# Performance work log

Hardware: AMD Instinct MI355X
Metric: run time of the kernel (lower is better)

Reference implementation:

```python
import jax, jax.numpy as jnp
import numpy as np

DIM = 192
SHIFT = 3
PAD = SHIFT // 2  # 1
EPS = 1e-5


def conv1x1(x, w, b):
    # 1x1x1 Conv3d == channel matmul. x: (B,C,D,H,W), w: (O,C), b: (O,)
    return jnp.einsum('bcdhw,oc->bodhw', x, w) + b[None, :, None, None, None]


def group_norm1(x, w, b):
    # GroupNorm(1, C): normalize over (C,D,H,W) per sample, per-channel affine.
    mu = x.mean(axis=(1, 2, 3, 4), keepdims=True)
    var = x.var(axis=(1, 2, 3, 4), keepdims=True)
    xn = (x - mu) * jax.lax.rsqrt(var + EPS)
    return xn * w[None, :, None, None, None] + b[None, :, None, None, None]


def axial_shift(x, axis):
    # reflect-pad all 3 spatial dims, roll channel-chunks along `axis`, crop back.
    R = x.shape[-1]
    xp = jnp.pad(x, ((0, 0), (0, 0), (PAD, PAD), (PAD, PAD), (PAD, PAD)), mode='reflect')
    chunks = jnp.split(xp, SHIFT, axis=1)
    rolled = [jnp.roll(c, s, axis=axis) for c, s in zip(chunks, range(-PAD, PAD + 1))]
    xc = jnp.concatenate(rolled, axis=1)
    return xc[:, :, PAD:PAD + R, PAD:PAD + R, PAD:PAD + R]


def setup_inputs() -> dict:
    key = jax.random.key(0)
    ks = jax.random.split(key, 16)
    B, C, R = 8, DIM, 32
    x = jax.random.normal(ks[0], (B, C, R, R, R), dtype=jnp.float32)
    wmat = lambda k: jax.random.normal(k, (C, C), dtype=jnp.float32) * 0.05
    vec = lambda k: jax.random.normal(k, (C,), dtype=jnp.float32) * 0.05
    return {
        'x': x,
        'w1': wmat(ks[1]), 'b1': vec(ks[2]),
        'n1w': jnp.ones((C,), jnp.float32), 'n1b': jnp.zeros((C,), jnp.float32),
        'w21': wmat(ks[3]), 'b21': vec(ks[4]),
        'w22': wmat(ks[5]), 'b22': vec(ks[6]),
        'w23': wmat(ks[7]), 'b23': vec(ks[8]),
        'n2w': jnp.ones((C,), jnp.float32), 'n2b': jnp.zeros((C,), jnp.float32),
        'w3': wmat(ks[9]), 'b3': vec(ks[10]),
    }


def reference(x, w1, b1, n1w, n1b, w21, b21, w22, b22, w23, b23, n2w, n2b, w3, b3):
    h = conv1x1(x, w1, b1)
    h = group_norm1(h, n1w, n1b)
    h = jax.nn.gelu(h, approximate=False)
    h = axial_shift(h, axis=3)
    h = conv1x1(h, w22, b22)
    h = axial_shift(h, axis=2)
    h = conv1x1(h, w21, b21)
    h = axial_shift(h, axis=4)
    h = conv1x1(h, w23, b23)
    h = jax.nn.gelu(h, approximate=False)
    h = group_norm1(h, n2w, n2b)
    h = conv1x1(h, w3, b3)
    return h
```

## Files before the change

kernel.cpp:

```cpp
#include <hip/hip_runtime.h>
#include <math.h>

#define NCH 192
#define NB 8
#define SPAT 32768
#define TILES_PER_B 512
#define NBLK (NB * TILES_PER_B)
#define NELEM_PER_B ((size_t)NCH * SPAT)

typedef short s16x8 __attribute__((ext_vector_type(8)));
typedef float f32x4 __attribute__((ext_vector_type(4)));

__device__ __forceinline__ float bf2f(unsigned short h) {
  return __uint_as_float(((unsigned)h) << 16);
}
__device__ __forceinline__ unsigned short f2bf(float f) {
  unsigned u = __float_as_uint(f);
  u += 0x7FFF + ((u >> 16) & 1);
  return (unsigned short)(u >> 16);
}
__device__ __forceinline__ unsigned cvt_pk(float lo, float hi) {
  unsigned r;
  asm("v_cvt_pk_bf16_f32 %0, %1, %2" : "=v"(r) : "v"(lo), "v"(hi));
  return r;
}

__device__ __forceinline__ float gelu_f(float x) {
  float x2 = x * x;
  float z2 = x * fmaf(x2, 0.0713548163f, 1.5957769100f);
  float e = __expf(z2);
  float r = __builtin_amdgcn_rcpf(e + 1.0f);
  return fmaf(-r, x, x);
}

__device__ __forceinline__ int rshift(int i, int c) {
  int j = i - (c - 1);
  j = (j < 0) ? 1 : j;
  j = (j > 31) ? 30 : j;
  return j;
}

__device__ __forceinline__ int lds_off(int c, int p, int u) {
  return (c * 64 + p) * 128 + 16 * (((u >> 3) ^ (p & 7) ^ ((p >> 3) & 7)) & 7) + 2 * (u & 7);
}

template <int SHIFTW>
__device__ __forceinline__ void do_gemm48(const char* __restrict__ B,
                                          const unsigned short* __restrict__ wm,
                                          int wave, int col, int kg,
                                          f32x4 acc[3][4]) {
  const unsigned short* wp = wm + (wave * 48 + col) * NCH + kg * 8;
  s16x8 afc[3], afn[3];
#pragma unroll
  for (int r = 0; r < 3; ++r) afc[r] = *(const s16x8*)(wp + r * 16 * NCH);
#pragma unroll
  for (int ks = 0; ks < 6; ++ks) {
    if (ks < 5) {
#pragma unroll
      for (int r = 0; r < 3; ++r)
        afn[r] = *(const s16x8*)(wp + (ks + 1) * 32 + r * 16 * NCH);
    }
    int k0 = ks * 32 + kg * 8;
    int c = k0 >> 6, u = k0 & 63;
    s16x8 bf[4];
#pragma unroll
    for (int m = 0; m < 4; ++m) {
      int p = m * 16 + col;
      int ps = SHIFTW ? ((p & 32) | rshift(p & 31, c)) : p;
      bf[m] = *(const s16x8*)(B + lds_off(c, ps, u));
    }
#pragma unroll
    for (int r = 0; r < 3; ++r)
#pragma unroll
      for (int m = 0; m < 4; ++m)
        acc[r][m] = __builtin_amdgcn_mfma_f32_16x16x32_bf16(afc[r], bf[m], acc[r][m], 0, 0, 0);
#pragma unroll
    for (int r = 0; r < 3; ++r) afc[r] = afn[r];
  }
}

__device__ __forceinline__ void stats_reduce(float ssum, float ssq, int wave, int lane,
                                             float* red, float* partials, int blk) {
#pragma unroll
  for (int off = 1; off < 64; off <<= 1) {
    ssum += __shfl_xor(ssum, off, 64);
    ssq += __shfl_xor(ssq, off, 64);
  }
  if (lane == 0) { red[wave * 2] = ssum; red[wave * 2 + 1] = ssq; }
  __syncthreads();
  if (wave == 0 && lane == 0) {
    partials[blk * 2] = red[0] + red[2] + red[4] + red[6];
    partials[blk * 2 + 1] = red[1] + red[3] + red[5] + red[7];
  }
}

__device__ __forceinline__ void store_tile(const char* __restrict__ L, char* __restrict__ ob,
                                           int tid) {
  int G = tid & 7;
#pragma unroll
  for (int j = 0; j < 6; ++j) {
    const int c = j >> 1;
    int p = (j & 1) * 32 + (tid >> 3);
    s16x8 v = *(const s16x8*)(L + lds_off(c, p, G * 8));
    *(s16x8*)(ob + (size_t)p * 384 + (c * 8 + G) * 16) = v;
  }
}

__global__ __launch_bounds__(256, 4)
void pass1(const float* __restrict__ x, const unsigned short* __restrict__ w1b,
           const float* __restrict__ b1, unsigned short* __restrict__ out,
           float* __restrict__ partials) {
  __shared__ __align__(16) char B[3 * 64 * 128];
  __shared__ float red[8];
  int blk = blockIdx.x, b = blk >> 9, p0 = (blk & 511) * 64;
  int tid = threadIdx.x, wave = tid >> 6, lane = tid & 63;
  int col = lane & 15, kg = lane >> 4;

  const float* xb = x + (size_t)b * NELEM_PER_B + p0;
  int q = tid & 15;
#pragma unroll
  for (int j = 0; j < 6; ++j) {
    int chp = j * 16 + (tid >> 4);
    int ch0 = 2 * chp;
    int cc = chp >> 5, u0 = ch0 & 63;
    const float* s0 = xb + (size_t)ch0 * SPAT + 4 * q;
    f32x4 a = *(const f32x4*)s0;
    f32x4 c2 = *(const f32x4*)(s0 + SPAT);
#pragma unroll
    for (int i = 0; i < 4; ++i)
      *(unsigned*)(B + lds_off(cc, 4 * q + i, u0)) = cvt_pk(a[i], c2[i]);
  }
  __syncthreads();

  f32x4 acc[3][4] = {};
  do_gemm48<0>(B, w1b, wave, col, kg, acc);

  float ssum = 0.f, ssq = 0.f;
  __syncthreads();
#pragma unroll
  for (int r = 0; r < 3; ++r) {
    int rowb = wave * 48 + r * 16 + kg * 4;
    f32x4 bs = *(const f32x4*)(b1 + rowb);
#pragma unroll
    for (int m = 0; m < 4; ++m) {
      int p = m * 16 + col;
      float v0 = acc[r][m][0] + bs[0], v1 = acc[r][m][1] + bs[1];
      float v2 = acc[r][m][2] + bs[2], v3 = acc[r][m][3] + bs[3];
      ssum += (v0 + v1) + (v2 + v3);
      ssq = fmaf(v0, v0, fmaf(v1, v1, fmaf(v2, v2, fmaf(v3, v3, ssq))));
      uint2 pk; pk.x = cvt_pk(v0, v1); pk.y = cvt_pk(v2, v3);
      *(uint2*)(B + lds_off(rowb >> 6, p, rowb & 63)) = pk;
    }
  }
  __syncthreads();
  store_tile(B, (char*)out + ((size_t)b * SPAT + p0) * 384, tid);
  stats_reduce(ssum, ssq, wave, lane, red, partials, blk);
}

__global__ __launch_bounds__(256, 4)
void pass2a(const unsigned short* __restrict__ in, const unsigned short* __restrict__ w22b,
            const float* __restrict__ b22, unsigned short* __restrict__ out,
            const unsigned short* __restrict__ ACbf) {
  __shared__ __align__(16) char B[3 * 64 * 128];
  int blk = blockIdx.x, b = blk >> 9, p0 = (blk & 511) * 64;
  int tid = threadIdx.x, wave = tid >> 6, lane = tid & 63;
  int col = lane & 15, kg = lane >> 4;

  const char* ib = (const char*)in + (size_t)b * SPAT * 384;
  const unsigned short* acb = ACbf + b * 2 * NCH;
  int G = tid & 7;
#pragma unroll
  for (int j = 0; j < 6; ++j) {
    const int c = j >> 1;
    int p = (j & 1) * 32 + (tid >> 3);
    int h = ((p0 + p) >> 5) & 31;
    int sp = (p0 + p) + (rshift(h, c) - h) * 32;
    s16x8 v = *(const s16x8*)(ib + (size_t)sp * 384 + (c * 8 + G) * 16);
    s16x8 aA = *(const s16x8*)(acb + c * 64 + G * 8);
    s16x8 aC = *(const s16x8*)(acb + NCH + c * 64 + G * 8);
    unsigned w[4];
#pragma unroll
    for (int i = 0; i < 4; ++i) {
      float f0 = gelu_f(fmaf(bf2f((unsigned short)v[2 * i]), bf2f((unsigned short)aA[2 * i]),
                             bf2f((unsigned short)aC[2 * i])));
      float f1 = gelu_f(fmaf(bf2f((unsigned short)v[2 * i + 1]), bf2f((unsigned short)aA[2 * i + 1]),
                             bf2f((unsigned short)aC[2 * i + 1])));
      w[i] = cvt_pk(f0, f1);
    }
    *(uint2*)(B + lds_off(c, p, G * 8)) = make_uint2(w[0], w[1]);
    *(uint2*)(B + lds_off(c, p, G * 8 + 4)) = make_uint2(w[2], w[3]);
  }
  __syncthreads();

  f32x4 acc[3][4] = {};
  do_gemm48<0>(B, w22b, wave, col, kg, acc);
  __syncthreads();
#pragma unroll
  for (int r = 0; r < 3; ++r) {
    int rowb = wave * 48 + r * 16 + kg * 4;
    f32x4 bs = *(const f32x4*)(b22 + rowb);
#pragma unroll
    for (int m = 0; m < 4; ++m) {
      int p = m * 16 + col;
      uint2 pk;
      pk.x = cvt_pk(acc[r][m][0] + bs[0], acc[r][m][1] + bs[1]);
      pk.y = cvt_pk(acc[r][m][2] + bs[2], acc[r][m][3] + bs[3]);
      *(uint2*)(B + lds_off(rowb >> 6, p, rowb & 63)) = pk;
    }
  }
  __syncthreads();
  store_tile(B, (char*)out + ((size_t)b * SPAT + p0) * 384, tid);
}

__global__ __launch_bounds__(256, 4)
void pass2bc(const unsigned short* __restrict__ in, const unsigned short* __restrict__ w21b,
             const float* __restrict__ b21, const unsigned short* __restrict__ w23b,
             const float* __restrict__ b23, unsigned short* __restrict__ out,
             float* __restrict__ partials) {
  __shared__ __align__(16) char B[3 * 64 * 128];
  __shared__ float red[8];
  int blk = blockIdx.x, b = blk >> 9, p0 = (blk & 511) * 64;
  int tid = threadIdx.x, wave = tid >> 6, lane = tid & 63;
  int col = lane & 15, kg = lane >> 4;

  int d = p0 >> 10;
  int soff[3];
#pragma unroll
  for (int c = 0; c < 3; ++c) soff[c] = (rshift(d, c) - d) * 1024;

  const char* ib = (const char*)in + (size_t)b * SPAT * 384;
  int G = tid & 7;
#pragma unroll
  for (int j = 0; j < 6; ++j) {
    const int c = j >> 1;
    int p = (j & 1) * 32 + (tid >> 3);
    s16x8 v = *(const s16x8*)(ib + (size_t)(p0 + p + soff[c]) * 384 + (c * 8 + G) * 16);
    *(s16x8*)(B + lds_off(c, p, G * 8)) = v;
  }
  __syncthreads();

  f32x4 acc[3][4] = {};
  do_gemm48<0>(B, w21b, wave, col, kg, acc);
  __syncthreads();
#pragma unroll
  for (int r = 0; r < 3; ++r) {
    int rowb = wave * 48 + r * 16 + kg * 4;
    f32x4 bs = *(const f32x4*)(b21 + rowb);
#pragma unroll
    for (int m = 0; m < 4; ++m) {
      int p = m * 16 + col;
      uint2 pk;
      pk.x = cvt_pk(acc[r][m][0] + bs[0], acc[r][m][1] + bs[1]);
      pk.y = cvt_pk(acc[r][m][2] + bs[2], acc[r][m][3] + bs[3]);
      *(uint2*)(B + lds_off(rowb >> 6, p, rowb & 63)) = pk;
    }
  }
  __syncthreads();

#pragma unroll
  for (int r = 0; r < 3; ++r)
#pragma unroll
    for (int m = 0; m < 4; ++m) acc[r][m] = (f32x4){0.f, 0.f, 0.f, 0.f};
  do_gemm48<1>(B, w23b, wave, col, kg, acc);
  __syncthreads();

  float ssum = 0.f, ssq = 0.f;
#pragma unroll
  for (int r = 0; r < 3; ++r) {
    int rowb = wave * 48 + r * 16 + kg * 4;
    f32x4 bs = *(const f32x4*)(b23 + rowb);
#pragma unroll
    for (int m = 0; m < 4; ++m) {
      int p = m * 16 + col;
      float v0 = gelu_f(acc[r][m][0] + bs[0]), v1 = gelu_f(acc[r][m][1] + bs[1]);
      float v2 = gelu_f(acc[r][m][2] + bs[2]), v3 = gelu_f(acc[r][m][3] + bs[3]);
      ssum += (v0 + v1) + (v2 + v3);
      ssq = fmaf(v0, v0, fmaf(v1, v1, fmaf(v2, v2, fmaf(v3, v3, ssq))));
      uint2 pk; pk.x = cvt_pk(v0, v1); pk.y = cvt_pk(v2, v3);
      *(uint2*)(B + lds_off(rowb >> 6, p, rowb & 63)) = pk;
    }
  }
  __syncthreads();
  store_tile(B, (char*)out + ((size_t)b * SPAT + p0) * 384, tid);
  stats_reduce(ssum, ssq, wave, lane, red, partials, blk);
}

__global__ __launch_bounds__(256, 4)
void pass3(const unsigned short* __restrict__ in, const unsigned short* __restrict__ w3e,
           const float* __restrict__ b3e, float* __restrict__ outf) {
  __shared__ __align__(16) char B[3 * 64 * 128];
  int blk = blockIdx.x, b = blk >> 9, p0 = (blk & 511) * 64;
  int tid = threadIdx.x, wave = tid >> 6, lane = tid & 63;
  int col = lane & 15, kg = lane >> 4;

  const char* ib = (const char*)in + (size_t)b * SPAT * 384;
  int G = tid & 7;
#pragma unroll
  for (int j = 0; j < 6; ++j) {
    const int c = j >> 1;
    int p = (j & 1) * 32 + (tid >> 3);
    s16x8 v = *(const s16x8*)(ib + (size_t)(p0 + p) * 384 + (c * 8 + G) * 16);
    *(s16x8*)(B + lds_off(c, p, G * 8)) = v;
  }
  __syncthreads();

  f32x4 acc[3][4] = {};
  do_gemm48<0>(B, w3e + (size_t)b * NCH * NCH, wave, col, kg, acc);

  const float* bb = b3e + b * NCH;
#pragma unroll
  for (int r = 0; r < 3; ++r) {
    int rowb = wave * 48 + r * 16 + kg * 4;
    f32x4 bs = *(const f32x4*)(bb + rowb);
#pragma unroll
    for (int m = 0; m < 4; ++m) {
      int p = p0 + m * 16 + col;
#pragma unroll
      for (int j = 0; j < 4; ++j)
        outf[((size_t)b * NCH + rowb + j) * SPAT + p] = acc[r][m][j] + bs[j];
    }
  }
}

__global__ void stats_finalize(const float* __restrict__ partials,
                               const float* __restrict__ nw, const float* __restrict__ nb,
                               float* __restrict__ AC, unsigned short* __restrict__ ACbf) {
  int b = blockIdx.x, tid = threadIdx.x;
  __shared__ float s0[256], s1[256];
  float a = 0.f, c = 0.f;
  for (int i = tid; i < TILES_PER_B; i += 256) {
    a += partials[(b * TILES_PER_B + i) * 2];
    c += partials[(b * TILES_PER_B + i) * 2 + 1];
  }
  s0[tid] = a; s1[tid] = c;
  __syncthreads();
  for (int st = 128; st > 0; st >>= 1) {
    if (tid < st) { s0[tid] += s0[tid + st]; s1[tid] += s1[tid + st]; }
    __syncthreads();
  }
  float inv_n = 1.0f / (float)NELEM_PER_B;
  float mu = s0[0] * inv_n;
  float var = s1[0] * inv_n - mu * mu;
  float rs = rsqrtf(var + 1e-5f);
  if (tid < NCH) {
    float A = rs * nw[tid];
    float C = nb[tid] - mu * A;
    AC[b * 2 * NCH + tid] = A;
    AC[b * 2 * NCH + NCH + tid] = C;
    ACbf[b * 2 * NCH + tid] = f2bf(A);
    ACbf[b * 2 * NCH + NCH + tid] = f2bf(C);
  }
}

__global__ void prep_weights(const float* __restrict__ w1, const float* __restrict__ w21,
                             const float* __restrict__ w22, const float* __restrict__ w23,
                             unsigned short* __restrict__ wb) {
  int i = blockIdx.x * 256 + threadIdx.x;
  if (i >= 4 * NCH * NCH) return;
  int m = i / (NCH * NCH), r = i % (NCH * NCH);
  const float* src = (m == 0) ? w1 : (m == 1) ? w22 : (m == 2) ? w21 : w23;
  wb[i] = f2bf(src[r]);
}

__global__ void prep_w3(const float* __restrict__ w3, const float* __restrict__ b3,
                        const float* __restrict__ AC2,
                        unsigned short* __restrict__ w3e, float* __restrict__ b3e) {
  int b = blockIdx.x, o = threadIdx.x;
  if (o >= NCH) return;
  const float* A = AC2 + b * 2 * NCH;
  const float* C = A + NCH;
  float s = b3[o];
  for (int c = 0; c < NCH; ++c) {
    float w = w3[o * NCH + c];
    w3e[((size_t)b * NCH + o) * NCH + c] = f2bf(w * A[c]);
    s = fmaf(w, C[c], s);
  }
  b3e[b * NCH + o] = s;
}

extern "C" void kernel_launch(void* const* d_in, const int* in_sizes, int n_in,
                              void* d_out, int out_size, void* d_ws, size_t ws_size,
                              hipStream_t stream) {
  const float* x   = (const float*)d_in[0];
  const float* w1  = (const float*)d_in[1];
  const float* b1  = (const float*)d_in[2];
  const float* n1w = (const float*)d_in[3];
  const float* n1b = (const float*)d_in[4];
  const float* w21 = (const float*)d_in[5];
  const float* b21 = (const float*)d_in[6];
  const float* w22 = (const float*)d_in[7];
  const float* b22 = (const float*)d_in[8];
  const float* w23 = (const float*)d_in[9];
  const float* b23 = (const float*)d_in[10];
  const float* n2w = (const float*)d_in[11];
  const float* n2b = (const float*)d_in[12];
  const float* w3  = (const float*)d_in[13];
  const float* b3  = (const float*)d_in[14];

  char* ws = (char*)d_ws;
  size_t off = 0;
  unsigned short* wb = (unsigned short*)(ws + off); off += (size_t)4 * NCH * NCH * 2;
  off = (off + 255) & ~(size_t)255;
  unsigned short* w3e = (unsigned short*)(ws + off); off += (size_t)NB * NCH * NCH * 2;
  off = (off + 255) & ~(size_t)255;
  float* b3e = (float*)(ws + off); off += NB * NCH * 4;
  float* AC1 = (float*)(ws + off); off += NB * 2 * NCH * 4;
  float* AC2 = (float*)(ws + off); off += NB * 2 * NCH * 4;
  unsigned short* ACbf1 = (unsigned short*)(ws + off); off += NB * 2 * NCH * 2;
  unsigned short* ACbf2 = (unsigned short*)(ws + off); off += NB * 2 * NCH * 2;
  off = (off + 255) & ~(size_t)255;
  float* part1 = (float*)(ws + off); off += (size_t)NBLK * 2 * 4;
  float* part2 = (float*)(ws + off); off += (size_t)NBLK * 2 * 4;
  off = (off + 255) & ~(size_t)255;
  unsigned short* R1 = (unsigned short*)(ws + off);
  unsigned short* R2 = (unsigned short*)d_out;

  prep_weights<<<(4 * NCH * NCH + 255) / 256, 256, 0, stream>>>(w1, w21, w22, w23, wb);

  pass1<<<NBLK, 256, 0, stream>>>(x, wb + 0 * NCH * NCH, b1, R1, part1);
  stats_finalize<<<NB, 256, 0, stream>>>(part1, n1w, n1b, AC1, ACbf1);

  pass2a<<<NBLK, 256, 0, stream>>>(R1, wb + 1 * NCH * NCH, b22, R2, ACbf1);

  pass2bc<<<NBLK, 256, 0, stream>>>(R2, wb + 2 * NCH * NCH, b21,
                                    wb + 3 * NCH * NCH, b23, R1, part2);
  stats_finalize<<<NB, 256, 0, stream>>>(part2, n2w, n2b, AC2, ACbf2);
  prep_w3<<<NB, NCH, 0, stream>>>(w3, b3, AC2, w3e, b3e);

  pass3<<<NBLK, 256, 0, stream>>>(R1, w3e, b3e, (float*)d_out);
}
```

Measured before the change: 334.5 us.

## Process four tiles per block with register-prefetched, double-buffered LDS pipeline

The shift/GEMM passes (2a, 2bc, 3) are merged into one templated persistent-style kernel, and pass3 gets the same treatment. Each block now handles four 64-voxel tiles and loads the next tile's global data into registers while the current tile's MFMA GEMM runs, using two LDS buffers and custom barriers. The aim is to hide global load latency and cut block launch and tail overhead. In exchange the grid is four times smaller, LDS per block doubles, and the launch-bounds occupancy hint of 4 is dropped, so fewer waves may be resident.

```diff
diff --git a/kernel.cpp b/kernel.cpp
--- a/kernel.cpp
+++ b/kernel.cpp
@@ -5,7 +5,9 @@
 #define NB 8
 #define SPAT 32768
 #define TILES_PER_B 512
-#define NBLK (NB * TILES_PER_B)
+#define NBLK1 (NB * TILES_PER_B)
+#define TPW 4
+#define NBLKP (NB * (TILES_PER_B / TPW))
 #define NELEM_PER_B ((size_t)NCH * SPAT)
 
 typedef short s16x8 __attribute__((ext_vector_type(8)));
@@ -42,6 +44,21 @@
 
 __device__ __forceinline__ int lds_off(int c, int p, int u) {
   return (c * 64 + p) * 128 + 16 * (((u >> 3) ^ (p & 7) ^ ((p >> 3) & 7)) & 7) + 2 * (u & 7);
+}
+
+__device__ __forceinline__ void bar_lgkm() {
+  __builtin_amdgcn_sched_barrier(0);
+  asm volatile("s_waitcnt lgkmcnt(0)" ::: "memory");
+  __builtin_amdgcn_s_barrier();
+  asm volatile("" ::: "memory");
+  __builtin_amdgcn_sched_barrier(0);
+}
+__device__ __forceinline__ void bar_plain() {
+  __builtin_amdgcn_sched_barrier(0);
+  asm volatile("" ::: "memory");
+  __builtin_amdgcn_s_barrier();
+  asm volatile("" ::: "memory");
+  __builtin_amdgcn_sched_barrier(0);
 }
 
 template <int SHIFTW>
@@ -79,6 +96,62 @@
   }
 }
 
+template <int AX>
+__device__ __forceinline__ void stage_load(const char* __restrict__ ib, int p0, int tid,
+                                           s16x8 vr[6]) {
+#pragma unroll
+  for (int j = 0; j < 6; ++j) {
+    const int c = j >> 1;
+    int p = (j & 1) * 32 + (tid >> 3);
+    int G = tid & 7;
+    int pp = p0 + p, sp;
+    if (AX == 0) sp = pp;
+    else if (AX == 3) { int h = (pp >> 5) & 31; sp = pp + (rshift(h, c) - h) * 32; }
+    else            { int d = pp >> 10;       sp = pp + (rshift(d, c) - d) * 1024; }
+    vr[j] = *(const s16x8*)(ib + (size_t)sp * 384 + (c * 8 + G) * 16);
+  }
+}
+
+template <int FUSE>
+__device__ __forceinline__ void stage_write(char* __restrict__ B, int tid, const s16x8 vr[6],
+                                            const unsigned short* __restrict__ acb) {
+#pragma unroll
+  for (int j = 0; j < 6; ++j) {
+    const int c = j >> 1;
+    int p = (j & 1) * 32 + (tid >> 3);
+    int G = tid & 7;
+    if (FUSE) {
+      s16x8 aA = *(const s16x8*)(acb + c * 64 + G * 8);
+      s16x8 aC = *(const s16x8*)(acb + NCH + c * 64 + G * 8);
+      unsigned w[4];
+#pragma unroll
+      for (int i = 0; i < 4; ++i) {
+        float f0 = gelu_f(fmaf(bf2f((unsigned short)vr[j][2 * i]), bf2f((unsigned short)aA[2 * i]),
+                               bf2f((unsigned short)aC[2 * i])));
+        float f1 = gelu_f(fmaf(bf2f((unsigned short)vr[j][2 * i + 1]), bf2f((unsigned short)aA[2 * i + 1]),
+                               bf2f((unsigned short)aC[2 * i + 1])));
+        w[i] = cvt_pk(f0, f1);
+      }
+      *(uint2*)(B + lds_off(c, p, G * 8)) = make_uint2(w[0], w[1]);
+      *(uint2*)(B + lds_off(c, p, G * 8 + 4)) = make_uint2(w[2], w[3]);
+    } else {
+      *(s16x8*)(B + lds_off(c, p, G * 8)) = vr[j];
+    }
+  }
+}
+
+__device__ __forceinline__ void store_tile(const char* __restrict__ L, char* __restrict__ ob,
+                                           int tid) {
+  int G = tid & 7;
+#pragma unroll
+  for (int j = 0; j < 6; ++j) {
+    const int c = j >> 1;
+    int p = (j & 1) * 32 + (tid >> 3);
+    s16x8 v = *(const s16x8*)(L + lds_off(c, p, G * 8));
+    *(s16x8*)(ob + (size_t)p * 384 + (c * 8 + G) * 16) = v;
+  }
+}
+
 __device__ __forceinline__ void stats_reduce(float ssum, float ssq, int wave, int lane,
                                              float* red, float* partials, int blk) {
 #pragma unroll
@@ -91,18 +164,6 @@
   if (wave == 0 && lane == 0) {
     partials[blk * 2] = red[0] + red[2] + red[4] + red[6];
     partials[blk * 2 + 1] = red[1] + red[3] + red[5] + red[7];
-  }
-}
-
-__device__ __forceinline__ void store_tile(const char* __restrict__ L, char* __restrict__ ob,
-                                           int tid) {
-  int G = tid & 7;
-#pragma unroll
-  for (int j = 0; j < 6; ++j) {
-    const int c = j >> 1;
-    int p = (j & 1) * 32 + (tid >> 3);
-    s16x8 v = *(const s16x8*)(L + lds_off(c, p, G * 8));
-    *(s16x8*)(ob + (size_t)p * 384 + (c * 8 + G) * 16) = v;
   }
 }
 
@@ -157,180 +218,141 @@
   stats_reduce(ssum, ssq, wave, lane, red, partials, blk);
 }
 
-__global__ __launch_bounds__(256, 4)
-void pass2a(const unsigned short* __restrict__ in, const unsigned short* __restrict__ w22b,
-            const float* __restrict__ b22, unsigned short* __restrict__ out,
-            const unsigned short* __restrict__ ACbf) {
-  __shared__ __align__(16) char B[3 * 64 * 128];
-  int blk = blockIdx.x, b = blk >> 9, p0 = (blk & 511) * 64;
+template <int AX, int FUSE, int CHAIN, int EPI2>
+__global__ __launch_bounds__(256)
+void pipe_pass(const unsigned short* __restrict__ in, const unsigned short* __restrict__ wA,
+               const float* __restrict__ bA, const unsigned short* __restrict__ wB,
+               const float* __restrict__ bB, unsigned short* __restrict__ out,
+               float* __restrict__ partials, const unsigned short* __restrict__ ACbf) {
+  __shared__ __align__(16) char buf[2][3 * 64 * 128];
+  __shared__ float red[8];
+  int blk = blockIdx.x, b = blk / (TILES_PER_B / TPW);
+  int ti0 = (blk % (TILES_PER_B / TPW)) * TPW;
   int tid = threadIdx.x, wave = tid >> 6, lane = tid & 63;
   int col = lane & 15, kg = lane >> 4;
 
   const char* ib = (const char*)in + (size_t)b * SPAT * 384;
-  const unsigned short* acb = ACbf + b * 2 * NCH;
-  int G = tid & 7;
-#pragma unroll
-  for (int j = 0; j < 6; ++j) {
-    const int c = j >> 1;
-    int p = (j & 1) * 32 + (tid >> 3);
-    int h = ((p0 + p) >> 5) & 31;
-    int sp = (p0 + p) + (rshift(h, c) - h) * 32;
-    s16x8 v = *(const s16x8*)(ib + (size_t)sp * 384 + (c * 8 + G) * 16);
-    s16x8 aA = *(const s16x8*)(acb + c * 64 + G * 8);
-    s16x8 aC = *(const s16x8*)(acb + NCH + c * 64 + G * 8);
-    unsigned w[4];
-#pragma unroll
-    for (int i = 0; i < 4; ++i) {
-      float f0 = gelu_f(fmaf(bf2f((unsigned short)v[2 * i]), bf2f((unsigned short)aA[2 * i]),
-                             bf2f((unsigned short)aC[2 * i])));
-      float f1 = gelu_f(fmaf(bf2f((unsigned short)v[2 * i + 1]), bf2f((unsigned short)aA[2 * i + 1]),
-                             bf2f((unsigned short)aC[2 * i + 1])));
-      w[i] = cvt_pk(f0, f1);
-    }
-    *(uint2*)(B + lds_off(c, p, G * 8)) = make_uint2(w[0], w[1]);
-    *(uint2*)(B + lds_off(c, p, G * 8 + 4)) = make_uint2(w[2], w[3]);
-  }
-  __syncthreads();
-
-  f32x4 acc[3][4] = {};
-  do_gemm48<0>(B, w22b, wave, col, kg, acc);
-  __syncthreads();
-#pragma unroll
-  for (int r = 0; r < 3; ++r) {
-    int rowb = wave * 48 + r * 16 + kg * 4;
-    f32x4 bs = *(const f32x4*)(b22 + rowb);
-#pragma unroll
-    for (int m = 0; m < 4; ++m) {
-      int p = m * 16 + col;
-      uint2 pk;
-      pk.x = cvt_pk(acc[r][m][0] + bs[0], acc[r][m][1] + bs[1]);
-      pk.y = cvt_pk(acc[r][m][2] + bs[2], acc[r][m][3] + bs[3]);
-      *(uint2*)(B + lds_off(rowb >> 6, p, rowb & 63)) = pk;
-    }
-  }
-  __syncthreads();
-  store_tile(B, (char*)out + ((size_t)b * SPAT + p0) * 384, tid);
-}
-
-__global__ __launch_bounds__(256, 4)
-void pass2bc(const unsigned short* __restrict__ in, const unsigned short* __restrict__ w21b,
-             const float* __restrict__ b21, const unsigned short* __restrict__ w23b,
-             const float* __restrict__ b23, unsigned short* __restrict__ out,
-             float* __restrict__ partials) {
-  __shared__ __align__(16) char B[3 * 64 * 128];
-  __shared__ float red[8];
-  int blk = blockIdx.x, b = blk >> 9, p0 = (blk & 511) * 64;
+  const unsigned short* acb = FUSE ? (ACbf + b * 2 * NCH) : nullptr;
+  float ssum = 0.f, ssq = 0.f;
+
+  s16x8 vr[6];
+  stage_load<AX>(ib, ti0 * 64, tid, vr);
+
+#pragma unroll
+  for (int t = 0; t < TPW; ++t) {
+    char* W = buf[t & 1];
+    int p0 = (ti0 + t) * 64;
+
+    stage_write<FUSE>(W, tid, vr, acb);
+    if (t + 1 < TPW) stage_load<AX>(ib, (ti0 + t + 1) * 64, tid, vr);
+    bar_lgkm();
+
+    f32x4 acc[3][4] = {};
+    do_gemm48<0>(W, wA, wave, col, kg, acc);
+    bar_plain();
+
+    if constexpr (CHAIN) {
+#pragma unroll
+      for (int r = 0; r < 3; ++r) {
+        int rowb = wave * 48 + r * 16 + kg * 4;
+        f32x4 bs = *(const f32x4*)(bA + rowb);
+#pragma unroll
+        for (int m = 0; m < 4; ++m) {
+          int p = m * 16 + col;
+          uint2 pk;
+          pk.x = cvt_pk(acc[r][m][0] + bs[0], acc[r][m][1] + bs[1]);
+          pk.y = cvt_pk(acc[r][m][2] + bs[2], acc[r][m][3] + bs[3]);
+          *(uint2*)(W + lds_off(rowb >> 6, p, rowb & 63)) = pk;
+        }
+      }
+      bar_lgkm();
+#pragma unroll
+      for (int r = 0; r < 3; ++r)
+#pragma unroll
+        for (int m = 0; m < 4; ++m) acc[r][m] = (f32x4){0.f, 0.f, 0.f, 0.f};
+      do_gemm48<1>(W, wB, wave, col, kg, acc);
+      bar_plain();
+    }
+
+    const float* bfin = CHAIN ? bB : bA;
+#pragma unroll
+    for (int r = 0; r < 3; ++r) {
+      int rowb = wave * 48 + r * 16 + kg * 4;
+      f32x4 bs = *(const f32x4*)(bfin + rowb);
+#pragma unroll
+      for (int m = 0; m < 4; ++m) {
+        int p = m * 16 + col;
+        float v0 = acc[r][m][0] + bs[0], v1 = acc[r][m][1] + bs[1];
+        float v2 = acc[r][m][2] + bs[2], v3 = acc[r][m][3] + bs[3];
+        if (EPI2) {
+          v0 = gelu_f(v0); v1 = gelu_f(v1); v2 = gelu_f(v2); v3 = gelu_f(v3);
+          ssum += (v0 + v1) + (v2 + v3);
+          ssq = fmaf(v0, v0, fmaf(v1, v1, fmaf(v2, v2, fmaf(v3, v3, ssq))));
+        }
+        uint2 pk; pk.x = cvt_pk(v0, v1); pk.y = cvt_pk(v2, v3);
+        *(uint2*)(W + lds_off(rowb >> 6, p, rowb & 63)) = pk;
+      }
+    }
+    bar_lgkm();
+    store_tile(W, (char*)out + ((size_t)b * SPAT + p0) * 384, tid);
+  }
+
+  if (EPI2) stats_reduce(ssum, ssq, wave, lane, red, partials, blk);
+}
+
+__global__ __launch_bounds__(256)
+void pass3(const unsigned short* __restrict__ in, const unsigned short* __restrict__ w3e,
+           const float* __restrict__ b3e, float* __restrict__ outf) {
+  __shared__ __align__(16) char buf[2][3 * 64 * 128];
+  int blk = blockIdx.x, b = blk / (TILES_PER_B / TPW);
+  int ti0 = (blk % (TILES_PER_B / TPW)) * TPW;
   int tid = threadIdx.x, wave = tid >> 6, lane = tid & 63;
   int col = lane & 15, kg = lane >> 4;
 
-  int d = p0 >> 10;
-  int soff[3];
-#pragma unroll
-  for (int c = 0; c < 3; ++c) soff[c] = (rshift(d, c) - d) * 1024;
-
   const char* ib = (const char*)in + (size_t)b * SPAT * 384;
-  int G = tid & 7;
-#pragma unroll
-  for (int j = 0; j < 6; ++j) {
-    const int c = j >> 1;
-    int p = (j & 1) * 32 + (tid >> 3);
-    s16x8 v = *(const s16x8*)(ib + (size_t)(p0 + p + soff[c]) * 384 + (c * 8 + G) * 16);
-    *(s16x8*)(B + lds_off(c, p, G * 8)) = v;
-  }
-  __syncthreads();
-
-  f32x4 acc[3][4] = {};
-  do_gemm48<0>(B, w21b, wave, col, kg, acc);
-  __syncthreads();
-#pragma unroll
-  for (int r = 0; r < 3; ++r) {
-    int rowb = wave * 48 + r * 16 + kg * 4;
-    f32x4 bs = *(const f32x4*)(b21 + rowb);
-#pragma unroll
-    for (int m = 0; m < 4; ++m) {
-      int p = m * 16 + col;
-      uint2 pk;
-      pk.x = cvt_pk(acc[r][m][0] + bs[0], acc[r][m][1] + bs[1]);
-      pk.y = cvt_pk(acc[r][m][2] + bs[2], acc[r][m][3] + bs[3]);
-      *(uint2*)(B + lds_off(rowb >> 6, p, rowb & 63)) = pk;
-    }
-  }
-  __syncthreads();
-
-#pragma unroll
-  for (int r = 0; r < 3; ++r)
-#pragma unroll
-    for (int m = 0; m < 4; ++m) acc[r][m] = (f32x4){0.f, 0.f, 0.f, 0.f};
-  do_gemm48<1>(B, w23b, wave, col, kg, acc);
-  __syncthreads();
-
-  float ssum = 0.f, ssq = 0.f;
-#pragma unroll
-  for (int r = 0; r < 3; ++r) {
-    int rowb = wave * 48 + r * 16 + kg * 4;
-    f32x4 bs = *(const f32x4*)(b23 + rowb);
-#pragma unroll
-    for (int m = 0; m < 4; ++m) {
-      int p = m * 16 + col;
-      float v0 = gelu_f(acc[r][m][0] + bs[0]), v1 = gelu_f(acc[r][m][1] + bs[1]);
-      float v2 = gelu_f(acc[r][m][2] + bs[2]), v3 = gelu_f(acc[r][m][3] + bs[3]);
-      ssum += (v0 + v1) + (v2 + v3);
-      ssq = fmaf(v0, v0, fmaf(v1, v1, fmaf(v2, v2, fmaf(v3, v3, ssq))));
-      uint2 pk; pk.x = cvt_pk(v0, v1); pk.y = cvt_pk(v2, v3);
-      *(uint2*)(B + lds_off(rowb >> 6, p, rowb & 63)) = pk;
-    }
-  }
-  __syncthreads();
-  store_tile(B, (char*)out + ((size_t)b * SPAT + p0) * 384, tid);
-  stats_reduce(ssum, ssq, wave, lane, red, partials, blk);
-}
-
-__global__ __launch_bounds__(256, 4)
-void pass3(const unsigned short* __restrict__ in, const unsigned short* __restrict__ w3e,
-           const float* __restrict__ b3e, float* __restrict__ outf) {
-  __shared__ __align__(16) char B[3 * 64 * 128];
-  int blk = blockIdx.x, b = blk >> 9, p0 = (blk & 511) * 64;
-  int tid = threadIdx.x, wave = tid >> 6, lane = tid & 63;
-  int col = lane & 15, kg = lane >> 4;
-
-  const char* ib = (const char*)in + (size_t)b * SPAT * 384;
-  int G = tid & 7;
-#pragma unroll
-  for (int j = 0; j < 6; ++j) {
-    const int c = j >> 1;
-    int p = (j & 1) * 32 + (tid >> 3);
-    s16x8 v = *(const s16x8*)(ib + (size_t)(p0 + p) * 384 + (c * 8 + G) * 16);
-    *(s16x8*)(B + lds_off(c, p, G * 8)) = v;
-  }
-  __syncthreads();
-
-  f32x4 acc[3][4] = {};
-  do_gemm48<0>(B, w3e + (size_t)b * NCH * NCH, wave, col, kg, acc);
-
+  const unsigned short* wbase = w3e + (size_t)b * NCH * NCH;
   const float* bb = b3e + b * NCH;
-#pragma unroll
-  for (int r = 0; r < 3; ++r) {
-    int rowb = wave * 48 + r * 16 + kg * 4;
-    f32x4 bs = *(const f32x4*)(bb + rowb);
-#pragma unroll
-    for (int m = 0; m < 4; ++m) {
-      int p = p0 + m * 16 + col;
-#pragma unroll
-      for (int j = 0; j < 4; ++j)
-        outf[((size_t)b * NCH + rowb + j) * SPAT + p] = acc[r][m][j] + bs[j];
+
+  s16x8 vr[6];
+  stage_load<0>(ib, ti0 * 64, tid, vr);
+
+#pragma unroll
+  for (int t = 0; t < TPW; ++t) {
+    char* W = buf[t & 1];
+    int p0 = (ti0 + t) * 64;
+    stage_write<0>(W, tid, vr, nullptr);
+    if (t + 1 < TPW) stage_load<0>(ib, (ti0 + t + 1) * 64, tid, vr);
+    bar_lgkm();
+
+    f32x4 acc[3][4] = {};
+    do_gemm48<0>(W, wbase, wave, col, kg, acc);
+    bar_lgkm();
+
+#pragma unroll
+    for (int r = 0; r < 3; ++r) {
+      int rowb = wave * 48 + r * 16 + kg * 4;
+      f32x4 bs = *(const f32x4*)(bb + rowb);
+#pragma unroll
+      for (int m = 0; m < 4; ++m) {
+        int p = p0 + m * 16 + col;
+#pragma unroll
+        for (int j = 0; j < 4; ++j)
+          outf[((size_t)b * NCH + rowb + j) * SPAT + p] = acc[r][m][j] + bs[j];
+      }
     }
   }
 }
 
 __global__ void stats_finalize(const float* __restrict__ partials,
                                const float* __restrict__ nw, const float* __restrict__ nb,
-                               float* __restrict__ AC, unsigned short* __restrict__ ACbf) {
+                               float* __restrict__ AC, unsigned short* __restrict__ ACbf,
+                               int nper) {
   int b = blockIdx.x, tid = threadIdx.x;
   __shared__ float s0[256], s1[256];
   float a = 0.f, c = 0.f;
-  for (int i = tid; i < TILES_PER_B; i += 256) {
-    a += partials[(b * TILES_PER_B + i) * 2];
-    c += partials[(b * TILES_PER_B + i) * 2 + 1];
+  for (int i = tid; i < nper; i += 256) {
+    a += partials[(b * nper + i) * 2];
+    c += partials[(b * nper + i) * 2 + 1];
   }
   s0[tid] = a; s1[tid] = c;
   __syncthreads();
@@ -409,23 +431,24 @@
   unsigned short* ACbf1 = (unsigned short*)(ws + off); off += NB * 2 * NCH * 2;
   unsigned short* ACbf2 = (unsigned short*)(ws + off); off += NB * 2 * NCH * 2;
   off = (off + 255) & ~(size_t)255;
-  float* part1 = (float*)(ws + off); off += (size_t)NBLK * 2 * 4;
-  float* part2 = (float*)(ws + off); off += (size_t)NBLK * 2 * 4;
+  float* part1 = (float*)(ws + off); off += (size_t)NBLK1 * 2 * 4;
+  float* part2 = (float*)(ws + off); off += (size_t)NBLKP * 2 * 4;
   off = (off + 255) & ~(size_t)255;
   unsigned short* R1 = (unsigned short*)(ws + off);
   unsigned short* R2 = (unsigned short*)d_out;
 
   prep_weights<<<(4 * NCH * NCH + 255) / 256, 256, 0, stream>>>(w1, w21, w22, w23, wb);
 
-  pass1<<<NBLK, 256, 0, stream>>>(x, wb + 0 * NCH * NCH, b1, R1, part1);
-  stats_finalize<<<NB, 256, 0, stream>>>(part1, n1w, n1b, AC1, ACbf1);
-
-  pass2a<<<NBLK, 256, 0, stream>>>(R1, wb + 1 * NCH * NCH, b22, R2, ACbf1);
-
-  pass2bc<<<NBLK, 256, 0, stream>>>(R2, wb + 2 * NCH * NCH, b21,
-                                    wb + 3 * NCH * NCH, b23, R1, part2);
-  stats_finalize<<<NB, 256, 0, stream>>>(part2, n2w, n2b, AC2, ACbf2);
+  pass1<<<NBLK1, 256, 0, stream>>>(x, wb + 0 * NCH * NCH, b1, R1, part1);
+  stats_finalize<<<NB, 256, 0, stream>>>(part1, n1w, n1b, AC1, ACbf1, TILES_PER_B);
+
+  pipe_pass<3, 1, 0, 0><<<NBLKP, 256, 0, stream>>>(
+      R1, wb + 1 * NCH * NCH, b22, nullptr, nullptr, R2, nullptr, ACbf1);
+
+  pipe_pass<2, 0, 1, 1><<<NBLKP, 256, 0, stream>>>(
+      R2, wb + 2 * NCH * NCH, b21, wb + 3 * NCH * NCH, b23, R1, part2, nullptr);
+  stats_finalize<<<NB, 256, 0, stream>>>(part2, n2w, n2b, AC2, ACbf2, TILES_PER_B / TPW);
   prep_w3<<<NB, NCH, 0, stream>>>(w3, b3, AC2, w3e, b3e);
 
-  pass3<<<NBLK, 256, 0, stream>>>(R1, w3e, b3e, (float*)d_out);
-}
+  pass3<<<NBLKP, 256, 0, stream>>>(R1, w3e, b3e, (float*)d_out);
+}
```

New measurement: 343.4 us. 1.03x slower.

## Replace pass2a and pass3 with single-wave 16-pixel-tile GEMM kernel

Applied to the files above, without the earlier changes.

Introduces a templated single-wavefront kernel that processes 16 spatial positions per block, with all 192 output channels computed by one wave, and uses it in place of the 256-thread, 64-position pass2a and pass3 kernels. The aim is more, smaller blocks with no __syncthreads, for better latency hiding and finer load balance. In exchange, every wave re-reads the full 192x192 weight matrix from global or cache for only 16 columns, which greatly raises weight traffic per output. The fp32 output store in pass3 also becomes narrower (16 contiguous floats per row).

```diff
diff --git a/kernel.cpp b/kernel.cpp
--- a/kernel.cpp
+++ b/kernel.cpp
@@ -5,7 +5,8 @@
 #define NB 8
 #define SPAT 32768
 #define TILES_PER_B 512
-#define NBLK (NB * TILES_PER_B)
+#define NBLK1 (NB * TILES_PER_B)
+#define NTLP (NB * 2048)
 #define NELEM_PER_B ((size_t)NCH * SPAT)
 
 typedef short s16x8 __attribute__((ext_vector_type(8)));
@@ -42,6 +43,9 @@
 
 __device__ __forceinline__ int lds_off(int c, int p, int u) {
   return (c * 64 + p) * 128 + 16 * (((u >> 3) ^ (p & 7) ^ ((p >> 3) & 7)) & 7) + 2 * (u & 7);
+}
+__device__ __forceinline__ int lds_off16(int c, int p, int u) {
+  return (c * 16 + p) * 128 + 16 * (((u >> 3) ^ (p & 7) ^ ((p >> 3) & 7)) & 7) + 2 * (u & 7);
 }
 
 template <int SHIFTW>
@@ -79,21 +83,6 @@
   }
 }
 
-__device__ __forceinline__ void stats_reduce(float ssum, float ssq, int wave, int lane,
-                                             float* red, float* partials, int blk) {
-#pragma unroll
-  for (int off = 1; off < 64; off <<= 1) {
-    ssum += __shfl_xor(ssum, off, 64);
-    ssq += __shfl_xor(ssq, off, 64);
-  }
-  if (lane == 0) { red[wave * 2] = ssum; red[wave * 2 + 1] = ssq; }
-  __syncthreads();
-  if (wave == 0 && lane == 0) {
-    partials[blk * 2] = red[0] + red[2] + red[4] + red[6];
-    partials[blk * 2 + 1] = red[1] + red[3] + red[5] + red[7];
-  }
-}
-
 __device__ __forceinline__ void store_tile(const char* __restrict__ L, char* __restrict__ ob,
                                            int tid) {
   int G = tid & 7;
@@ -103,6 +92,21 @@
     int p = (j & 1) * 32 + (tid >> 3);
     s16x8 v = *(const s16x8*)(L + lds_off(c, p, G * 8));
     *(s16x8*)(ob + (size_t)p * 384 + (c * 8 + G) * 16) = v;
+  }
+}
+
+__device__ __forceinline__ void stats_reduce(float ssum, float ssq, int wave, int lane,
+                                             float* red, float* partials, int blk) {
+#pragma unroll
+  for (int off = 1; off < 64; off <<= 1) {
+    ssum += __shfl_xor(ssum, off, 64);
+    ssq += __shfl_xor(ssq, off, 64);
+  }
+  if (lane == 0) { red[wave * 2] = ssum; red[wave * 2 + 1] = ssq; }
+  __syncthreads();
+  if (wave == 0 && lane == 0) {
+    partials[blk * 2] = red[0] + red[2] + red[4] + red[6];
+    partials[blk * 2 + 1] = red[1] + red[3] + red[5] + red[7];
   }
 }
 
@@ -157,59 +161,100 @@
   stats_reduce(ssum, ssq, wave, lane, red, partials, blk);
 }
 
-__global__ __launch_bounds__(256, 4)
-void pass2a(const unsigned short* __restrict__ in, const unsigned short* __restrict__ w22b,
-            const float* __restrict__ b22, unsigned short* __restrict__ out,
-            const unsigned short* __restrict__ ACbf) {
-  __shared__ __align__(16) char B[3 * 64 * 128];
-  int blk = blockIdx.x, b = blk >> 9, p0 = (blk & 511) * 64;
-  int tid = threadIdx.x, wave = tid >> 6, lane = tid & 63;
-  int col = lane & 15, kg = lane >> 4;
+template <int AX, int FUSE, int PERB, int OUTF>
+__global__ __launch_bounds__(64, 4)
+void tlp_pass(const unsigned short* __restrict__ in,
+              const unsigned short* __restrict__ wmat,
+              const float* __restrict__ bias,
+              void* __restrict__ outv,
+              const unsigned short* __restrict__ ACbf) {
+  __shared__ __align__(16) char B[3 * 16 * 128];
+  int blk = blockIdx.x;
+  int b = blk >> 11;
+  int p0 = (blk & 2047) * 16;
+  int lane = threadIdx.x & 63;
+  int col = lane & 15, kg = lane >> 4, G = lane & 7;
 
   const char* ib = (const char*)in + (size_t)b * SPAT * 384;
-  const unsigned short* acb = ACbf + b * 2 * NCH;
-  int G = tid & 7;
+  const unsigned short* wbase = wmat + (PERB ? (size_t)b * NCH * NCH : 0);
+  const float* bbase = bias + (PERB ? b * NCH : 0);
+  const unsigned short* acb = FUSE ? (ACbf + b * 2 * NCH) : nullptr;
+
 #pragma unroll
   for (int j = 0; j < 6; ++j) {
     const int c = j >> 1;
-    int p = (j & 1) * 32 + (tid >> 3);
-    int h = ((p0 + p) >> 5) & 31;
-    int sp = (p0 + p) + (rshift(h, c) - h) * 32;
+    int p = (j & 1) * 8 + (lane >> 3);
+    int pp = p0 + p;
+    int sp = pp;
+    if (AX == 3) { int h = (pp >> 5) & 31; sp = pp + (rshift(h, c) - h) * 32; }
     s16x8 v = *(const s16x8*)(ib + (size_t)sp * 384 + (c * 8 + G) * 16);
-    s16x8 aA = *(const s16x8*)(acb + c * 64 + G * 8);
-    s16x8 aC = *(const s16x8*)(acb + NCH + c * 64 + G * 8);
-    unsigned w[4];
-#pragma unroll
-    for (int i = 0; i < 4; ++i) {
-      float f0 = gelu_f(fmaf(bf2f((unsigned short)v[2 * i]), bf2f((unsigned short)aA[2 * i]),
-                             bf2f((unsigned short)aC[2 * i])));
-      float f1 = gelu_f(fmaf(bf2f((unsigned short)v[2 * i + 1]), bf2f((unsigned short)aA[2 * i + 1]),
-                             bf2f((unsigned short)aC[2 * i + 1])));
-      w[i] = cvt_pk(f0, f1);
-    }
-    *(uint2*)(B + lds_off(c, p, G * 8)) = make_uint2(w[0], w[1]);
-    *(uint2*)(B + lds_off(c, p, G * 8 + 4)) = make_uint2(w[2], w[3]);
-  }
-  __syncthreads();
-
-  f32x4 acc[3][4] = {};
-  do_gemm48<0>(B, w22b, wave, col, kg, acc);
-  __syncthreads();
-#pragma unroll
-  for (int r = 0; r < 3; ++r) {
-    int rowb = wave * 48 + r * 16 + kg * 4;
-    f32x4 bs = *(const f32x4*)(b22 + rowb);
-#pragma unroll
-    for (int m = 0; m < 4; ++m) {
-      int p = m * 16 + col;
+    if (FUSE) {
+      s16x8 aA = *(const s16x8*)(acb + c * 64 + G * 8);
+      s16x8 aC = *(const s16x8*)(acb + NCH + c * 64 + G * 8);
+      unsigned w[4];
+#pragma unroll
+      for (int i = 0; i < 4; ++i) {
+        float f0 = gelu_f(fmaf(bf2f((unsigned short)v[2 * i]),
+                               bf2f((unsigned short)aA[2 * i]),
+                               bf2f((unsigned short)aC[2 * i])));
+        float f1 = gelu_f(fmaf(bf2f((unsigned short)v[2 * i + 1]),
+                               bf2f((unsigned short)aA[2 * i + 1]),
+                               bf2f((unsigned short)aC[2 * i + 1])));
+        w[i] = cvt_pk(f0, f1);
+      }
+      *(uint2*)(B + lds_off16(c, p, G * 8)) = make_uint2(w[0], w[1]);
+      *(uint2*)(B + lds_off16(c, p, G * 8 + 4)) = make_uint2(w[2], w[3]);
+    } else {
+      *(s16x8*)(B + lds_off16(c, p, G * 8)) = v;
+    }
+  }
+
+  f32x4 acc[12] = {};
+#pragma unroll
+  for (int rb = 0; rb < 2; ++rb) {
+#pragma unroll
+    for (int ks = 0; ks < 6; ++ks) {
+      int k0 = ks * 32 + kg * 8;
+      int c = k0 >> 6, u = k0 & 63;
+      s16x8 bf = *(const s16x8*)(B + lds_off16(c, col, u));
+#pragma unroll
+      for (int rr = 0; rr < 6; ++rr) {
+        int r = rb * 6 + rr;
+        s16x8 af = *(const s16x8*)(wbase + (r * 16 + col) * NCH + k0);
+        acc[r] = __builtin_amdgcn_mfma_f32_16x16x32_bf16(af, bf, acc[r], 0, 0, 0);
+      }
+    }
+  }
+
+  if (OUTF == 0) {
+#pragma unroll
+    for (int r = 0; r < 12; ++r) {
+      int rowb = r * 16 + kg * 4;
+      f32x4 bs = *(const f32x4*)(bbase + rowb);
       uint2 pk;
-      pk.x = cvt_pk(acc[r][m][0] + bs[0], acc[r][m][1] + bs[1]);
-      pk.y = cvt_pk(acc[r][m][2] + bs[2], acc[r][m][3] + bs[3]);
-      *(uint2*)(B + lds_off(rowb >> 6, p, rowb & 63)) = pk;
-    }
-  }
-  __syncthreads();
-  store_tile(B, (char*)out + ((size_t)b * SPAT + p0) * 384, tid);
+      pk.x = cvt_pk(acc[r][0] + bs[0], acc[r][1] + bs[1]);
+      pk.y = cvt_pk(acc[r][2] + bs[2], acc[r][3] + bs[3]);
+      *(uint2*)(B + lds_off16(rowb >> 6, col, rowb & 63)) = pk;
+    }
+    char* ob = (char*)outv + ((size_t)b * SPAT + p0) * 384;
+#pragma unroll
+    for (int j = 0; j < 6; ++j) {
+      const int c = j >> 1;
+      int p = (j & 1) * 8 + (lane >> 3);
+      s16x8 v = *(const s16x8*)(B + lds_off16(c, p, G * 8));
+      *(s16x8*)(ob + (size_t)p * 384 + (c * 8 + G) * 16) = v;
+    }
+  } else {
+    float* outf = (float*)outv;
+#pragma unroll
+    for (int r = 0; r < 12; ++r) {
+      int rowb = r * 16 + kg * 4;
+      f32x4 bs = *(const f32x4*)(bbase + rowb);
+#pragma unroll
+      for (int j = 0; j < 4; ++j)
+        outf[((size_t)b * NCH + rowb + j) * SPAT + p0 + col] = acc[r][j] + bs[j];
+    }
+  }
 }
 
 __global__ __launch_bounds__(256, 4)
@@ -285,52 +330,16 @@
   stats_reduce(ssum, ssq, wave, lane, red, partials, blk);
 }
 
-__global__ __launch_bounds__(256, 4)
-void pass3(const unsigned short* __restrict__ in, const unsigned short* __restrict__ w3e,
-           const float* __restrict__ b3e, float* __restrict__ outf) {
-  __shared__ __align__(16) char B[3 * 64 * 128];
-  int blk = blockIdx.x, b = blk >> 9, p0 = (blk & 511) * 64;
-  int tid = threadIdx.x, wave = tid >> 6, lane = tid & 63;
-  int col = lane & 15, kg = lane >> 4;
-
-  const char* ib = (const char*)in + (size_t)b * SPAT * 384;
-  int G = tid & 7;
-#pragma unroll
-  for (int j = 0; j < 6; ++j) {
-    const int c = j >> 1;
-    int p = (j & 1) * 32 + (tid >> 3);
-    s16x8 v = *(const s16x8*)(ib + (size_t)(p0 + p) * 384 + (c * 8 + G) * 16);
-    *(s16x8*)(B + lds_off(c, p, G * 8)) = v;
-  }
-  __syncthreads();
-
-  f32x4 acc[3][4] = {};
-  do_gemm48<0>(B, w3e + (size_t)b * NCH * NCH, wave, col, kg, acc);
-
-  const float* bb = b3e + b * NCH;
-#pragma unroll
-  for (int r = 0; r < 3; ++r) {
-    int rowb = wave * 48 + r * 16 + kg * 4;
-    f32x4 bs = *(const f32x4*)(bb + rowb);
-#pragma unroll
-    for (int m = 0; m < 4; ++m) {
-      int p = p0 + m * 16 + col;
-#pragma unroll
-      for (int j = 0; j < 4; ++j)
-        outf[((size_t)b * NCH + rowb + j) * SPAT + p] = acc[r][m][j] + bs[j];
-    }
-  }
-}
-
 __global__ void stats_finalize(const float* __restrict__ partials,
                                const float* __restrict__ nw, const float* __restrict__ nb,
-                               float* __restrict__ AC, unsigned short* __restrict__ ACbf) {
+                               float* __restrict__ AC, unsigned short* __restrict__ ACbf,
+                               int nper) {
   int b = blockIdx.x, tid = threadIdx.x;
   __shared__ float s0[256], s1[256];
   float a = 0.f, c = 0.f;
-  for (int i = tid; i < TILES_PER_B; i += 256) {
-    a += partials[(b * TILES_PER_B + i) * 2];
-    c += partials[(b * TILES_PER_B + i) * 2 + 1];
+  for (int i = tid; i < nper; i += 256) {
+    a += partials[(b * nper + i) * 2];
+    c += partials[(b * nper + i) * 2 + 1];
   }
   s0[tid] = a; s1[tid] = c;
   __syncthreads();
@@ -409,23 +418,25 @@
   unsigned short* ACbf1 = (unsigned short*)(ws + off); off += NB * 2 * NCH * 2;
   unsigned short* ACbf2 = (unsigned short*)(ws + off); off += NB * 2 * NCH * 2;
   off = (off + 255) & ~(size_t)255;
-  float* part1 = (float*)(ws + off); off += (size_t)NBLK * 2 * 4;
-  float* part2 = (float*)(ws + off); off += (size_t)NBLK * 2 * 4;
+  float* part1 = (float*)(ws + off); off += (size_t)NBLK1 * 2 * 4;
+  float* part2 = (float*)(ws + off); off += (size_t)NBLK1 * 2 * 4;
   off = (off + 255) & ~(size_t)255;
   unsigned short* R1 = (unsigned short*)(ws + off);
   unsigned short* R2 = (unsigned short*)d_out;
 
   prep_weights<<<(4 * NCH * NCH + 255) / 256, 256, 0, stream>>>(w1, w21, w22, w23, wb);
 
-  pass1<<<NBLK, 256, 0, stream>>>(x, wb + 0 * NCH * NCH, b1, R1, part1);
-  stats_finalize<<<NB, 256, 0, stream>>>(part1, n1w, n1b, AC1, ACbf1);
-
-  pass2a<<<NBLK, 256, 0, stream>>>(R1, wb + 1 * NCH * NCH, b22, R2, ACbf1);
-
-  pass2bc<<<NBLK, 256, 0, stream>>>(R2, wb + 2 * NCH * NCH, b21,
-                                    wb + 3 * NCH * NCH, b23, R1, part2);
-  stats_finalize<<<NB, 256, 0, stream>>>(part2, n2w, n2b, AC2, ACbf2);
+  pass1<<<NBLK1, 256, 0, stream>>>(x, wb + 0 * NCH * NCH, b1, R1, part1);
+  stats_finalize<<<NB, 256, 0, stream>>>(part1, n1w, n1b, AC1, ACbf1, TILES_PER_B);
+
+  tlp_pass<3, 1, 0, 0><<<NTLP, 64, 0, stream>>>(
+      R1, wb + 1 * NCH * NCH, b22, R2, ACbf1);
+
+  pass2bc<<<NBLK1, 256, 0, stream>>>(R2, wb + 2 * NCH * NCH, b21,
+                                     wb + 3 * NCH * NCH, b23, R1, part2);
+  stats_finalize<<<NB, 256, 0, stream>>>(part2, n2w, n2b, AC2, ACbf2, TILES_PER_B);
   prep_w3<<<NB, NCH, 0, stream>>>(w3, b3, AC2, w3e, b3e);
 
-  pass3<<<NBLK, 256, 0, stream>>>(R1, w3e, b3e, (float*)d_out);
-}
+  tlp_pass<0, 0, 1, 1><<<NTLP, 64, 0, stream>>>(
+      R1, w3e, b3e, (float*)d_out, nullptr);
+}
```

New measurement: 506.9 us. 51.6% more time.
